# Kernel optimization log

Hardware: AMD Instinct MI355X
Metric: run time of the kernel (lower is better)

The kernel has to match this reference:

```python
import jax, jax.numpy as jnp
import numpy as np

N_NODES = 50000
N_EDGES = 800000
D_IN = 128
D_OUT = 128
ALPHA = 0.2  # LeakyReLU negative slope


def setup_inputs() -> dict:
    key = jax.random.key(0)
    k1, k2, k3, k4 = jax.random.split(key, 4)
    x = jax.random.normal(k1, (N_NODES, D_IN), dtype=jnp.float32)
    W = jax.random.normal(k2, (D_IN, D_OUT), dtype=jnp.float32) * (1.414 / np.sqrt(D_IN))
    a = jax.random.normal(k3, (2 * D_OUT, 1), dtype=jnp.float32) * 0.1
    edge_index = jax.random.randint(k4, (2, N_EDGES), 0, N_NODES, dtype=jnp.int64)
    return {"x": x, "W": W, "a": a, "edge_index": edge_index}


def reference(x, W, a, edge_index):
    # h: (N, D_OUT)
    h = x @ W
    src, dst = edge_index[0], edge_index[1]
    # e_i = leakyrelu([h[src]; h[dst]] @ a) == leakyrelu((h@a1)[src] + (h@a2)[dst])
    a1 = a[:D_OUT, 0]
    a2 = a[D_OUT:, 0]
    s1 = h @ a1  # (N,)
    s2 = h @ a2  # (N,)
    e = jax.nn.leaky_relu(s1[src] + s2[dst], negative_slope=ALPHA)  # (E,)
    # Global softmax over all edges (faithful to F.softmax(edge_e, dim=0))
    attention = jax.nn.softmax(e)  # (E,)
    # output[dst] += attention * h[src]  (scatter-add)
    msgs = attention[:, None] * h[src]  # (E, D_OUT)
    output = jax.ops.segment_sum(msgs, dst, num_segments=N_NODES)
    return output
```

## Files before the change

kernel.cpp:

```cpp
#include <hip/hip_runtime.h>
#include <hip/hip_bf16.h>

#define N_NODES 50000
#define N_EDGES 800000
#define D 128
#define ALPHA 0.2f
#define NEG_INF -1e30f

#define KB_BLOCKS 3125
#define NSCAN_BLOCKS ((N_NODES + 255) / 256)
#define LDS_STRIDE 272

typedef __attribute__((ext_vector_type(8))) short short8;
typedef __attribute__((ext_vector_type(4))) float floatx4;

__device__ __forceinline__ unsigned int f2bf(float v)
{
    __hip_bfloat16 b = __float2bfloat16(v);
    return (unsigned int)*reinterpret_cast<unsigned short*>(&b);
}
__device__ __forceinline__ float bf_lo(unsigned int u)
{
    return __uint_as_float(u << 16);
}
__device__ __forceinline__ float bf_hi(unsigned int u)
{
    return __uint_as_float(u & 0xFFFF0000u);
}

__global__ __launch_bounds__(256) void k_prep(
    const float* __restrict__ W, const float* __restrict__ a,
    float* __restrict__ w12, int* __restrict__ deg)
{
    const int i = blockIdx.x * 256 + threadIdx.x;
    if (i < N_NODES) deg[i] = 0;
    if (blockIdx.x == 0) {
        const int t = threadIdx.x;
        const int r = t & 127;
        const int which = t >> 7;
        const float* av = a + which * D;
        float acc = 0.f;
        #pragma unroll 8
        for (int j = 0; j < D; ++j)
            acc += W[(size_t)r * D + j] * av[j];
        w12[which * D + r] = acc;
    }
}

__global__ __launch_bounds__(256) void k_fused(
    const float* __restrict__ x, const float* __restrict__ W,
    const float* __restrict__ w12, const int* __restrict__ ei,
    unsigned short* __restrict__ hb, float* __restrict__ s1,
    float* __restrict__ s2, int* __restrict__ deg, int* __restrict__ rank)
{
    __shared__ unsigned char lds[16 * LDS_STRIDE];
    const int t = threadIdx.x;
    const int rowbase = blockIdx.x * 16;

    const int r = t >> 4;
    const int c = t & 15;
    const float* xp = x + (size_t)(rowbase + r) * D + c * 8;
    const float4 v0 = *(const float4*)(xp);
    const float4 v1 = *(const float4*)(xp + 4);

    const int lane = t & 63;
    const int wv = t >> 6;
    const int q = lane >> 4;
    const int nIdx = lane & 15;
    const int n0 = wv * 32;
    short8 B[2][4];
    #pragma unroll
    for (int kt = 0; kt < 4; ++kt) {
        short8 be, bo;
        #pragma unroll
        for (int j = 0; j < 8; ++j) {
            const float* wp = W + (size_t)(kt * 32 + q * 8 + j) * D + n0 + 2 * nIdx;
            be[j] = (short)f2bf(wp[0]);
            bo[j] = (short)f2bf(wp[1]);
        }
        B[0][kt] = be;
        B[1][kt] = bo;
    }

    {
        const float* w1 = w12 + c * 8;
        const float* w2 = w12 + D + c * 8;
        float p1 = v0.x * w1[0] + v0.y * w1[1] + v0.z * w1[2] + v0.w * w1[3]
                 + v1.x * w1[4] + v1.y * w1[5] + v1.z * w1[6] + v1.w * w1[7];
        float p2 = v0.x * w2[0] + v0.y * w2[1] + v0.z * w2[2] + v0.w * w2[3]
                 + v1.x * w2[4] + v1.y * w2[5] + v1.z * w2[6] + v1.w * w2[7];
        #pragma unroll
        for (int mask = 8; mask >= 1; mask >>= 1) {
            p1 += __shfl_xor(p1, mask);
            p2 += __shfl_xor(p2, mask);
        }
        if (c == 0) { s1[rowbase + r] = p1; s2[rowbase + r] = p2; }

        uint4 pk;
        pk.x = f2bf(v0.x) | (f2bf(v0.y) << 16);
        pk.y = f2bf(v0.z) | (f2bf(v0.w) << 16);
        pk.z = f2bf(v1.x) | (f2bf(v1.y) << 16);
        pk.w = f2bf(v1.z) | (f2bf(v1.w) << 16);
        *(uint4*)(lds + r * LDS_STRIDE + c * 16) = pk;
    }
    __syncthreads();

    const unsigned char* ab = lds + nIdx * LDS_STRIDE + q * 16;
    const short8 A0 = *(const short8*)(ab);
    const short8 A1 = *(const short8*)(ab + 64);
    const short8 A2 = *(const short8*)(ab + 128);
    const short8 A3 = *(const short8*)(ab + 192);

    floatx4 acc0 = {0.f, 0.f, 0.f, 0.f};
    floatx4 acc1 = {0.f, 0.f, 0.f, 0.f};
    acc0 = __builtin_amdgcn_mfma_f32_16x16x32_bf16(A0, B[0][0], acc0, 0, 0, 0);
    acc1 = __builtin_amdgcn_mfma_f32_16x16x32_bf16(A0, B[1][0], acc1, 0, 0, 0);
    acc0 = __builtin_amdgcn_mfma_f32_16x16x32_bf16(A1, B[0][1], acc0, 0, 0, 0);
    acc1 = __builtin_amdgcn_mfma_f32_16x16x32_bf16(A1, B[1][1], acc1, 0, 0, 0);
    acc0 = __builtin_amdgcn_mfma_f32_16x16x32_bf16(A2, B[0][2], acc0, 0, 0, 0);
    acc1 = __builtin_amdgcn_mfma_f32_16x16x32_bf16(A2, B[1][2], acc1, 0, 0, 0);
    acc0 = __builtin_amdgcn_mfma_f32_16x16x32_bf16(A3, B[0][3], acc0, 0, 0, 0);
    acc1 = __builtin_amdgcn_mfma_f32_16x16x32_bf16(A3, B[1][3], acc1, 0, 0, 0);

    #pragma unroll
    for (int i = 0; i < 4; ++i) {
        const int row = rowbase + q * 4 + i;
        const unsigned int pk = f2bf(acc0[i]) | (f2bf(acc1[i]) << 16);
        *(unsigned int*)(hb + (size_t)row * D + n0 + 2 * nIdx) = pk;
    }

    const int e = blockIdx.x * 256 + t;
    rank[e] = atomicAdd(&deg[ei[N_EDGES + e]], 1);
}

__device__ __forceinline__ void online_combine(float& m, float& s,
                                               float om, float os)
{
    float nm = fmaxf(m, om);
    s = s * __expf(m - nm) + os * __expf(om - nm);
    m = nm;
}

__global__ __launch_bounds__(256) void k_scan_a(
    const int* __restrict__ deg, int* __restrict__ partials)
{
    const int i = blockIdx.x * 256 + threadIdx.x;
    int v = (i < N_NODES) ? deg[i] : 0;
    #pragma unroll
    for (int off = 32; off >= 1; off >>= 1) v += __shfl_down(v, off);
    __shared__ int ws[4];
    if ((threadIdx.x & 63) == 0) ws[threadIdx.x >> 6] = v;
    __syncthreads();
    if (threadIdx.x == 0)
        partials[blockIdx.x] = ws[0] + ws[1] + ws[2] + ws[3];
}

__global__ __launch_bounds__(256) void k_scan_b(
    const int* __restrict__ partials, int* __restrict__ partialOffs,
    int* __restrict__ offs)
{
    __shared__ int sc[256];
    const int t = threadIdx.x;
    int v = (t < NSCAN_BLOCKS) ? partials[t] : 0;
    sc[t] = v;
    __syncthreads();
    #pragma unroll
    for (int off = 1; off < 256; off <<= 1) {
        int u = (t >= off) ? sc[t - off] : 0;
        __syncthreads();
        sc[t] += u;
        __syncthreads();
    }
    if (t < NSCAN_BLOCKS) partialOffs[t] = sc[t] - v;
    if (t == 255) offs[N_NODES] = sc[255];
}

__global__ __launch_bounds__(256) void k_scan_c(
    const int* __restrict__ deg, const int* __restrict__ partialOffs,
    int* __restrict__ offs)
{
    __shared__ int sc[256];
    const int t = threadIdx.x;
    const int i = blockIdx.x * 256 + t;
    const int v = (i < N_NODES) ? deg[i] : 0;
    sc[t] = v;
    __syncthreads();
    #pragma unroll
    for (int off = 1; off < 256; off <<= 1) {
        int u = (t >= off) ? sc[t - off] : 0;
        __syncthreads();
        sc[t] += u;
        __syncthreads();
    }
    if (i < N_NODES)
        offs[i] = partialOffs[blockIdx.x] + sc[t] - v;
}

__global__ __launch_bounds__(256) void k_bucket(
    const int* __restrict__ ei, const float* __restrict__ s1,
    const float* __restrict__ s2, const int* __restrict__ offs,
    const int* __restrict__ rank, unsigned int* __restrict__ csr,
    float* __restrict__ bm, float* __restrict__ bs)
{
    const int e = blockIdx.x * 256 + threadIdx.x;
    const int sN = ei[e];
    const int dN = ei[N_EDGES + e];
    csr[offs[dN] + rank[e]] = (unsigned int)sN;

    float v = s1[sN] + s2[dN];
    v = v > 0.f ? v : ALPHA * v;

    float m = v, s = 1.f;
    #pragma unroll
    for (int off = 32; off >= 1; off >>= 1) {
        float om = __shfl_down(m, off);
        float os = __shfl_down(s, off);
        online_combine(m, s, om, os);
    }
    __shared__ float rm[4], rs[4];
    const int wid = threadIdx.x >> 6;
    if ((threadIdx.x & 63) == 0) { rm[wid] = m; rs[wid] = s; }
    __syncthreads();
    if (threadIdx.x == 0) {
        #pragma unroll
        for (int w = 1; w < 4; ++w) online_combine(m, s, rm[w], rs[w]);
        bm[blockIdx.x] = m;
        bs[blockIdx.x] = s;
    }
}

__global__ __launch_bounds__(256) void k_reduce_mz(
    const float* __restrict__ bm, const float* __restrict__ bs,
    float* __restrict__ MZ)
{
    float m = NEG_INF, s = 0.f;
    for (int i = threadIdx.x; i < KB_BLOCKS; i += 256)
        online_combine(m, s, bm[i], bs[i]);
    #pragma unroll
    for (int off = 32; off >= 1; off >>= 1) {
        float om = __shfl_down(m, off);
        float os = __shfl_down(s, off);
        online_combine(m, s, om, os);
    }
    __shared__ float rm[4], rs[4];
    const int wid = threadIdx.x >> 6;
    if ((threadIdx.x & 63) == 0) { rm[wid] = m; rs[wid] = s; }
    __syncthreads();
    if (threadIdx.x == 0) {
        #pragma unroll
        for (int w = 1; w < 4; ++w) online_combine(m, s, rm[w], rs[w]);
        MZ[0] = m;
        MZ[1] = s;
    }
}

__global__ __launch_bounds__(256) void k_gather(
    const unsigned int* __restrict__ csr, const int* __restrict__ offs,
    const float* __restrict__ s1, const float* __restrict__ s2,
    const unsigned short* __restrict__ hb, const float* __restrict__ MZ,
    float* __restrict__ out)
{
    const int node = (blockIdx.x * blockDim.x + threadIdx.x) >> 6;
    if (node >= N_NODES) return;
    const int lane = threadIdx.x & 63;
    const float M = MZ[0];
    const float invZ = 1.0f / MZ[1];
    const float s2n = s2[node];
    const int beg = offs[node];
    const int end = offs[node + 1];

    float a0 = 0.f, a1 = 0.f, b0 = 0.f, b1 = 0.f;
    float c0 = 0.f, c1 = 0.f, d0 = 0.f, d1 = 0.f;
    float e0 = 0.f, e1 = 0.f, f0 = 0.f, f1 = 0.f;
    float g0 = 0.f, g1 = 0.f, h0 = 0.f, h1 = 0.f;

    for (int cb = beg; cb < end; cb += 64) {
        const int n = min(64, end - cb);
        const int srcl = (cb + lane < end) ? (int)csr[cb + lane] : 0;
        float v = s1[srcl] + s2n;
        v = v > 0.f ? v : ALPHA * v;
        const float attl = __expf(v - M) * invZ;

        int j = 0;
        for (; j + 7 < n; j += 8) {
            const int i0 = __shfl(srcl, j);
            const int i1 = __shfl(srcl, j + 1);
            const int i2 = __shfl(srcl, j + 2);
            const int i3 = __shfl(srcl, j + 3);
            const int i4 = __shfl(srcl, j + 4);
            const int i5 = __shfl(srcl, j + 5);
            const int i6 = __shfl(srcl, j + 6);
            const int i7 = __shfl(srcl, j + 7);
            const float w0 = __shfl(attl, j);
            const float w1 = __shfl(attl, j + 1);
            const float w2 = __shfl(attl, j + 2);
            const float w3 = __shfl(attl, j + 3);
            const float w4 = __shfl(attl, j + 4);
            const float w5 = __shfl(attl, j + 5);
            const float w6 = __shfl(attl, j + 6);
            const float w7 = __shfl(attl, j + 7);
            const unsigned int u0 = *(const unsigned int*)(hb + (size_t)i0 * D + lane * 2);
            const unsigned int u1 = *(const unsigned int*)(hb + (size_t)i1 * D + lane * 2);
            const unsigned int u2 = *(const unsigned int*)(hb + (size_t)i2 * D + lane * 2);
            const unsigned int u3 = *(const unsigned int*)(hb + (size_t)i3 * D + lane * 2);
            const unsigned int u4 = *(const unsigned int*)(hb + (size_t)i4 * D + lane * 2);
            const unsigned int u5 = *(const unsigned int*)(hb + (size_t)i5 * D + lane * 2);
            const unsigned int u6 = *(const unsigned int*)(hb + (size_t)i6 * D + lane * 2);
            const unsigned int u7 = *(const unsigned int*)(hb + (size_t)i7 * D + lane * 2);
            a0 += w0 * bf_lo(u0); a1 += w0 * bf_hi(u0);
            b0 += w1 * bf_lo(u1); b1 += w1 * bf_hi(u1);
            c0 += w2 * bf_lo(u2); c1 += w2 * bf_hi(u2);
            d0 += w3 * bf_lo(u3); d1 += w3 * bf_hi(u3);
            e0 += w4 * bf_lo(u4); e1 += w4 * bf_hi(u4);
            f0 += w5 * bf_lo(u5); f1 += w5 * bf_hi(u5);
            g0 += w6 * bf_lo(u6); g1 += w6 * bf_hi(u6);
            h0 += w7 * bf_lo(u7); h1 += w7 * bf_hi(u7);
        }
        for (; j + 3 < n; j += 4) {
            const int i0 = __shfl(srcl, j);
            const int i1 = __shfl(srcl, j + 1);
            const int i2 = __shfl(srcl, j + 2);
            const int i3 = __shfl(srcl, j + 3);
            const float w0 = __shfl(attl, j);
            const float w1 = __shfl(attl, j + 1);
            const float w2 = __shfl(attl, j + 2);
            const float w3 = __shfl(attl, j + 3);
            const unsigned int u0 = *(const unsigned int*)(hb + (size_t)i0 * D + lane * 2);
            const unsigned int u1 = *(const unsigned int*)(hb + (size_t)i1 * D + lane * 2);
            const unsigned int u2 = *(const unsigned int*)(hb + (size_t)i2 * D + lane * 2);
            const unsigned int u3 = *(const unsigned int*)(hb + (size_t)i3 * D + lane * 2);
            a0 += w0 * bf_lo(u0); a1 += w0 * bf_hi(u0);
            b0 += w1 * bf_lo(u1); b1 += w1 * bf_hi(u1);
            c0 += w2 * bf_lo(u2); c1 += w2 * bf_hi(u2);
            d0 += w3 * bf_lo(u3); d1 += w3 * bf_hi(u3);
        }
        for (; j < n; ++j) {
            const int i0 = __shfl(srcl, j);
            const float w0 = __shfl(attl, j);
            const unsigned int u0 = *(const unsigned int*)(hb + (size_t)i0 * D + lane * 2);
            a0 += w0 * bf_lo(u0); a1 += w0 * bf_hi(u0);
        }
    }
    float2 r;
    r.x = ((a0 + b0) + (c0 + d0)) + ((e0 + f0) + (g0 + h0));
    r.y = ((a1 + b1) + (c1 + d1)) + ((e1 + f1) + (g1 + h1));
    *(float2*)(out + (size_t)node * D + lane * 2) = r;
}

extern "C" void kernel_launch(void* const* d_in, const int* in_sizes, int n_in,
                              void* d_out, int out_size, void* d_ws, size_t ws_size,
                              hipStream_t stream)
{
    const float* x = (const float*)d_in[0];
    const float* W = (const float*)d_in[1];
    const float* a = (const float*)d_in[2];
    const int* ei = (const int*)d_in[3];
    float* out = (float*)d_out;

    char* wsb = (char*)d_ws;
    unsigned int* csr = (unsigned int*)wsb;
    unsigned short* hb = (unsigned short*)(wsb + (size_t)N_EDGES * 4);
    int* rank     = (int*)((char*)hb + (size_t)N_NODES * D * 2);
    float* s1     = (float*)(rank + N_EDGES);
    float* s2     = s1 + N_NODES;
    int*   deg    = (int*)(s2 + N_NODES);
    int*   offs   = deg + N_NODES;
    int*   partials    = offs + N_NODES + 1;
    int*   partialOffs = partials + NSCAN_BLOCKS;
    float* w12    = (float*)(partialOffs + NSCAN_BLOCKS);
    float* bm     = w12 + 2 * D;
    float* bs     = bm + KB_BLOCKS;
    float* MZ     = bs + KB_BLOCKS;

    k_prep<<<NSCAN_BLOCKS, 256, 0, stream>>>(W, a, w12, deg);
    k_fused<<<N_NODES / 16, 256, 0, stream>>>(x, W, w12, ei, hb, s1, s2,
                                              deg, rank);
    k_scan_a<<<NSCAN_BLOCKS, 256, 0, stream>>>(deg, partials);
    k_scan_b<<<1, 256, 0, stream>>>(partials, partialOffs, offs);
    k_scan_c<<<NSCAN_BLOCKS, 256, 0, stream>>>(deg, partialOffs, offs);
    k_bucket<<<KB_BLOCKS, 256, 0, stream>>>(ei, s1, s2, offs, rank, csr,
                                            bm, bs);
    k_reduce_mz<<<1, 256, 0, stream>>>(bm, bs, MZ);
    k_gather<<<(N_NODES * 64 + 255) / 256, 256, 0, stream>>>(
        csr, offs, s1, s2, hb, MZ, out);
}
```

Baseline: 182.6 us.

## Collapse scan, bucket and softmax-reduce kernels into fewer launches

Folds the w12 precompute into each block of the fused GEMM kernel. Replaces the three-kernel degree scan with a single 1024-thread block that sits alongside the edge max/sum reduction blocks in one launch. The CSR scatter and the final softmax reduction now share a single post kernel. The goal is to cut the kernel launch count from eight to five and the serialization that comes with it, at the cost of recomputing w12 in every GEMM block and running a serial single-block scan over padded arrays.

```diff
diff --git a/kernel.cpp b/kernel.cpp
--- a/kernel.cpp
+++ b/kernel.cpp
@@ -8,8 +8,11 @@
 #define NEG_INF -1e30f
 
 #define KB_BLOCKS 3125
-#define NSCAN_BLOCKS ((N_NODES + 255) / 256)
 #define LDS_STRIDE 272
+
+#define SCAN_PER 52
+#define SCAN_PAD (1024 * SCAN_PER)
+#define NB_MS ((N_EDGES + 1023) / 1024)
 
 typedef __attribute__((ext_vector_type(8))) short short8;
 typedef __attribute__((ext_vector_type(4))) float floatx4;
@@ -28,34 +31,33 @@
     return __uint_as_float(u & 0xFFFF0000u);
 }
 
-__global__ __launch_bounds__(256) void k_prep(
-    const float* __restrict__ W, const float* __restrict__ a,
-    float* __restrict__ w12, int* __restrict__ deg)
-{
-    const int i = blockIdx.x * 256 + threadIdx.x;
-    if (i < N_NODES) deg[i] = 0;
-    if (blockIdx.x == 0) {
-        const int t = threadIdx.x;
-        const int r = t & 127;
+__global__ __launch_bounds__(1024) void k_zero(int* __restrict__ deg)
+{
+    deg[blockIdx.x * 1024 + threadIdx.x] = 0;
+}
+
+__global__ __launch_bounds__(256) void k_fused(
+    const float* __restrict__ x, const float* __restrict__ W,
+    const float* __restrict__ a, const int* __restrict__ ei,
+    unsigned short* __restrict__ hb, float* __restrict__ s1,
+    float* __restrict__ s2, int* __restrict__ deg, int* __restrict__ rank)
+{
+    __shared__ unsigned char lds[16 * LDS_STRIDE];
+    __shared__ float w12s[2 * D];
+    const int t = threadIdx.x;
+    const int rowbase = blockIdx.x * 16;
+
+    {
+        const int wr_ = t & 127;
         const int which = t >> 7;
         const float* av = a + which * D;
+        const float* wrow = W + (size_t)wr_ * D;
         float acc = 0.f;
         #pragma unroll 8
         for (int j = 0; j < D; ++j)
-            acc += W[(size_t)r * D + j] * av[j];
-        w12[which * D + r] = acc;
-    }
-}
-
-__global__ __launch_bounds__(256) void k_fused(
-    const float* __restrict__ x, const float* __restrict__ W,
-    const float* __restrict__ w12, const int* __restrict__ ei,
-    unsigned short* __restrict__ hb, float* __restrict__ s1,
-    float* __restrict__ s2, int* __restrict__ deg, int* __restrict__ rank)
-{
-    __shared__ unsigned char lds[16 * LDS_STRIDE];
-    const int t = threadIdx.x;
-    const int rowbase = blockIdx.x * 16;
+            acc += wrow[j] * av[j];
+        w12s[which * D + wr_] = acc;
+    }
 
     const int r = t >> 4;
     const int c = t & 15;
@@ -82,9 +84,11 @@
         B[1][kt] = bo;
     }
 
+    __syncthreads();
+
     {
-        const float* w1 = w12 + c * 8;
-        const float* w2 = w12 + D + c * 8;
+        const float* w1 = w12s + c * 8;
+        const float* w2 = w12s + D + c * 8;
         float p1 = v0.x * w1[0] + v0.y * w1[1] + v0.z * w1[2] + v0.w * w1[3]
                  + v1.x * w1[4] + v1.y * w1[5] + v1.z * w1[6] + v1.w * w1[7];
         float p2 = v0.x * w2[0] + v0.y * w2[1] + v0.z * w2[2] + v0.w * w2[3]
@@ -141,116 +145,117 @@
     m = nm;
 }
 
-__global__ __launch_bounds__(256) void k_scan_a(
-    const int* __restrict__ deg, int* __restrict__ partials)
-{
-    const int i = blockIdx.x * 256 + threadIdx.x;
-    int v = (i < N_NODES) ? deg[i] : 0;
-    #pragma unroll
-    for (int off = 32; off >= 1; off >>= 1) v += __shfl_down(v, off);
-    __shared__ int ws[4];
-    if ((threadIdx.x & 63) == 0) ws[threadIdx.x >> 6] = v;
-    __syncthreads();
-    if (threadIdx.x == 0)
-        partials[blockIdx.x] = ws[0] + ws[1] + ws[2] + ws[3];
-}
-
-__global__ __launch_bounds__(256) void k_scan_b(
-    const int* __restrict__ partials, int* __restrict__ partialOffs,
-    int* __restrict__ offs)
-{
-    __shared__ int sc[256];
+__global__ __launch_bounds__(1024) void k_mid(
+    const int* __restrict__ ei, const float* __restrict__ s1,
+    const float* __restrict__ s2, const int* __restrict__ deg,
+    int* __restrict__ offs, float* __restrict__ bm, float* __restrict__ bs)
+{
     const int t = threadIdx.x;
-    int v = (t < NSCAN_BLOCKS) ? partials[t] : 0;
-    sc[t] = v;
-    __syncthreads();
-    #pragma unroll
-    for (int off = 1; off < 256; off <<= 1) {
-        int u = (t >= off) ? sc[t - off] : 0;
+    const int lane = t & 63;
+    const int wv = t >> 6;
+
+    if (blockIdx.x == 0) {
+        __shared__ int wsum[16];
+        const int base = t * SCAN_PER;
+        int4 v[13];
+        const int4* dp = (const int4*)(deg + base);
+        int s = 0;
+        #pragma unroll
+        for (int k = 0; k < 13; ++k) {
+            v[k] = dp[k];
+            s += v[k].x + v[k].y + v[k].z + v[k].w;
+        }
+        int inc = s;
+        #pragma unroll
+        for (int off = 1; off < 64; off <<= 1) {
+            int u = __shfl_up(inc, off);
+            if (lane >= off) inc += u;
+        }
+        if (lane == 63) wsum[wv] = inc;
         __syncthreads();
-        sc[t] += u;
+        if (wv == 0 && lane < 16) {
+            int wval = wsum[lane];
+            int winc = wval;
+            #pragma unroll
+            for (int off = 1; off < 16; off <<= 1) {
+                int u = __shfl_up(winc, off);
+                if (lane >= off) winc += u;
+            }
+            wsum[lane] = winc - wval;
+        }
         __syncthreads();
-    }
-    if (t < NSCAN_BLOCKS) partialOffs[t] = sc[t] - v;
-    if (t == 255) offs[N_NODES] = sc[255];
-}
-
-__global__ __launch_bounds__(256) void k_scan_c(
-    const int* __restrict__ deg, const int* __restrict__ partialOffs,
-    int* __restrict__ offs)
-{
-    __shared__ int sc[256];
-    const int t = threadIdx.x;
-    const int i = blockIdx.x * 256 + t;
-    const int v = (i < N_NODES) ? deg[i] : 0;
-    sc[t] = v;
-    __syncthreads();
-    #pragma unroll
-    for (int off = 1; off < 256; off <<= 1) {
-        int u = (t >= off) ? sc[t - off] : 0;
-        __syncthreads();
-        sc[t] += u;
-        __syncthreads();
-    }
-    if (i < N_NODES)
-        offs[i] = partialOffs[blockIdx.x] + sc[t] - v;
-}
-
-__global__ __launch_bounds__(256) void k_bucket(
-    const int* __restrict__ ei, const float* __restrict__ s1,
-    const float* __restrict__ s2, const int* __restrict__ offs,
-    const int* __restrict__ rank, unsigned int* __restrict__ csr,
-    float* __restrict__ bm, float* __restrict__ bs)
-{
-    const int e = blockIdx.x * 256 + threadIdx.x;
-    const int sN = ei[e];
-    const int dN = ei[N_EDGES + e];
-    csr[offs[dN] + rank[e]] = (unsigned int)sN;
-
-    float v = s1[sN] + s2[dN];
-    v = v > 0.f ? v : ALPHA * v;
-
-    float m = v, s = 1.f;
+        int run = wsum[wv] + (inc - s);
+        int4* op = (int4*)(offs + base);
+        #pragma unroll
+        for (int k = 0; k < 13; ++k) {
+            int4 o;
+            o.x = run;             run += v[k].x;
+            o.y = run;             run += v[k].y;
+            o.z = run;             run += v[k].z;
+            o.w = run;             run += v[k].w;
+            op[k] = o;
+        }
+        return;
+    }
+
+    const int e = (blockIdx.x - 1) * 1024 + t;
+    float m = NEG_INF, s = 0.f;
+    if (e < N_EDGES) {
+        const int sN = ei[e];
+        const int dN = ei[N_EDGES + e];
+        float vv = s1[sN] + s2[dN];
+        vv = vv > 0.f ? vv : ALPHA * vv;
+        m = vv;
+        s = 1.f;
+    }
     #pragma unroll
     for (int off = 32; off >= 1; off >>= 1) {
         float om = __shfl_down(m, off);
         float os = __shfl_down(s, off);
         online_combine(m, s, om, os);
     }
-    __shared__ float rm[4], rs[4];
-    const int wid = threadIdx.x >> 6;
-    if ((threadIdx.x & 63) == 0) { rm[wid] = m; rs[wid] = s; }
+    __shared__ float rm[16], rs[16];
+    if (lane == 0) { rm[wv] = m; rs[wv] = s; }
     __syncthreads();
-    if (threadIdx.x == 0) {
-        #pragma unroll
-        for (int w = 1; w < 4; ++w) online_combine(m, s, rm[w], rs[w]);
-        bm[blockIdx.x] = m;
-        bs[blockIdx.x] = s;
-    }
-}
-
-__global__ __launch_bounds__(256) void k_reduce_mz(
+    if (t == 0) {
+        #pragma unroll
+        for (int w = 1; w < 16; ++w) online_combine(m, s, rm[w], rs[w]);
+        bm[blockIdx.x - 1] = m;
+        bs[blockIdx.x - 1] = s;
+    }
+}
+
+__global__ __launch_bounds__(256) void k_post(
+    const int* __restrict__ ei, const int* __restrict__ offs,
+    const int* __restrict__ rank, unsigned int* __restrict__ csr,
     const float* __restrict__ bm, const float* __restrict__ bs,
     float* __restrict__ MZ)
 {
-    float m = NEG_INF, s = 0.f;
-    for (int i = threadIdx.x; i < KB_BLOCKS; i += 256)
-        online_combine(m, s, bm[i], bs[i]);
-    #pragma unroll
-    for (int off = 32; off >= 1; off >>= 1) {
-        float om = __shfl_down(m, off);
-        float os = __shfl_down(s, off);
-        online_combine(m, s, om, os);
-    }
-    __shared__ float rm[4], rs[4];
-    const int wid = threadIdx.x >> 6;
-    if ((threadIdx.x & 63) == 0) { rm[wid] = m; rs[wid] = s; }
-    __syncthreads();
-    if (threadIdx.x == 0) {
-        #pragma unroll
-        for (int w = 1; w < 4; ++w) online_combine(m, s, rm[w], rs[w]);
-        MZ[0] = m;
-        MZ[1] = s;
+    const int e = blockIdx.x * 256 + threadIdx.x;
+    const int sN = ei[e];
+    const int dN = ei[N_EDGES + e];
+    csr[offs[dN] + rank[e]] = (unsigned int)sN;
+
+    if (blockIdx.x == 0) {
+        float m = NEG_INF, s = 0.f;
+        for (int i = threadIdx.x; i < NB_MS; i += 256)
+            online_combine(m, s, bm[i], bs[i]);
+        #pragma unroll
+        for (int off = 32; off >= 1; off >>= 1) {
+            float om = __shfl_down(m, off);
+            float os = __shfl_down(s, off);
+            online_combine(m, s, om, os);
+        }
+        __shared__ float rm[4], rs[4];
+        const int wid = threadIdx.x >> 6;
+        if ((threadIdx.x & 63) == 0) { rm[wid] = m; rs[wid] = s; }
+        __syncthreads();
+        if (threadIdx.x == 0) {
+            #pragma unroll
+            for (int w = 1; w < 4; ++w) online_combine(m, s, rm[w], rs[w]);
+            MZ[0] = m;
+            MZ[1] = s;
+        }
     }
 }
 
@@ -364,23 +369,16 @@
     float* s1     = (float*)(rank + N_EDGES);
     float* s2     = s1 + N_NODES;
     int*   deg    = (int*)(s2 + N_NODES);
-    int*   offs   = deg + N_NODES;
-    int*   partials    = offs + N_NODES + 1;
-    int*   partialOffs = partials + NSCAN_BLOCKS;
-    float* w12    = (float*)(partialOffs + NSCAN_BLOCKS);
-    float* bm     = w12 + 2 * D;
-    float* bs     = bm + KB_BLOCKS;
-    float* MZ     = bs + KB_BLOCKS;
-
-    k_prep<<<NSCAN_BLOCKS, 256, 0, stream>>>(W, a, w12, deg);
-    k_fused<<<N_NODES / 16, 256, 0, stream>>>(x, W, w12, ei, hb, s1, s2,
+    int*   offs   = deg + SCAN_PAD;
+    float* bm     = (float*)(offs + SCAN_PAD);
+    float* bs     = bm + NB_MS;
+    float* MZ     = bs + NB_MS;
+
+    k_zero<<<SCAN_PAD / 1024, 1024, 0, stream>>>(deg);
+    k_fused<<<N_NODES / 16, 256, 0, stream>>>(x, W, a, ei, hb, s1, s2,
                                               deg, rank);
-    k_scan_a<<<NSCAN_BLOCKS, 256, 0, stream>>>(deg, partials);
-    k_scan_b<<<1, 256, 0, stream>>>(partials, partialOffs, offs);
-    k_scan_c<<<NSCAN_BLOCKS, 256, 0, stream>>>(deg, partialOffs, offs);
-    k_bucket<<<KB_BLOCKS, 256, 0, stream>>>(ei, s1, s2, offs, rank, csr,
-                                            bm, bs);
-    k_reduce_mz<<<1, 256, 0, stream>>>(bm, bs, MZ);
+    k_mid<<<NB_MS + 1, 1024, 0, stream>>>(ei, s1, s2, deg, offs, bm, bs);
+    k_post<<<KB_BLOCKS, 256, 0, stream>>>(ei, offs, rank, csr, bm, bs, MZ);
     k_gather<<<(N_NODES * 64 + 255) / 256, 256, 0, stream>>>(
         csr, offs, s1, s2, hb, MZ, out);
 }
```

After: 224.0 us. 22.7% more time.
